# Kernel optimization log

Hardware: AMD Instinct MI355X
Metric: run time of the kernel (lower is better)

The kernel has to match this reference:

```python
import jax, jax.numpy as jnp
import numpy as np

B, R, D, P = 32, 512, 256, 5532  # images, rois/image, feat dim, num_pids
NEG_INF = -1e30

def setup_inputs() -> dict:
    key = jax.random.key(0)
    k1, k2, k3 = jax.random.split(key, 3)
    inputs = jax.random.normal(k1, (B * R, D), dtype=jnp.float32)
    cls_scores = jax.random.uniform(k2, (B * R, 1), dtype=jnp.float32)
    roi_label = jax.random.randint(k3, (B, R), 0, P + 1)  # 0 = background -> label -1
    return {"inputs": inputs, "cls_scores": cls_scores, "roi_label": roi_label}

def reference(inputs, cls_scores, roi_label):
    x = (inputs * cls_scores).reshape(B, R, D)          # scale features by cls score
    label = roi_label - 1                               # [B,R], -1 = background
    valid = label >= 0                                  # keep labeled ROIs only
    lbl = jnp.where(valid, label, 0)

    # per-image per-pid mean prototypes via one segmented reduction
    seg = (jnp.arange(B)[:, None] * P + lbl).reshape(-1)             # [B*R]
    w = valid.reshape(-1).astype(x.dtype)
    sums = jax.ops.segment_sum(x.reshape(-1, D) * w[:, None], seg, num_segments=B * P)
    counts = jax.ops.segment_sum(w, seg, num_segments=B * P)          # [B*P]
    proto = sums / jnp.maximum(counts, 1.0)[:, None]
    proto = proto / jnp.maximum(jnp.linalg.norm(proto, axis=-1, keepdims=True), 1e-12)
    proto = jax.lax.stop_gradient(proto).reshape(B, P, D)            # .detach() in torch
    present = (counts > 0).reshape(B, P)                              # unique labels per image

    # project each ROI feature onto its image's prototypes
    logits = jnp.einsum('brd,bpd->brp', x, proto)                     # [B,R,P]
    logits = jnp.where(present[:, None, :], logits, NEG_INF)          # softmax over unique labels only
    logp = jax.nn.log_softmax(logits, axis=-1)
    nll = -jnp.take_along_axis(logp, lbl[..., None], axis=-1)[..., 0] # [B,R]
    nll = jnp.where(valid, nll, 0.0)
    n_valid = jnp.maximum(jnp.sum(valid).astype(x.dtype), 1.0)
    return jnp.sum(nll) / n_valid
```

## Files before the change

kernel.cpp:

```cpp
#include <hip/hip_runtime.h>
#include <math.h>

#define Bn 32
#define Rn 512
#define Dn 256
#define Pn 5532
#define MAXU 512
#define NEGBIG -3.0e38f

typedef short short8 __attribute__((ext_vector_type(8)));
typedef short short4v __attribute__((ext_vector_type(4)));
typedef float floatx4 __attribute__((ext_vector_type(4)));

#define XBF_OFF    0
#define XBF_WORDS  (Bn*Rn*Dn/2)
#define PBF_OFF    (XBF_OFF + XBF_WORDS)
#define PBF_WORDS  (Bn*MAXU*Dn/2)
#define CMAP_OFF   (PBF_OFF + PBF_WORDS)
#define CCNT_OFF   (CMAP_OFF + Bn*Pn)
#define CURS_OFF   (CCNT_OFF + Bn*MAXU)
#define RLIST_OFF  (CURS_OFF + Bn*MAXU)
#define NUNIQ_OFF  (RLIST_OFF + Bn*Rn)
#define NVALID_OFF (NUNIQ_OFF + 32)
#define NLL_OFF    (NVALID_OFF + 32)
#define TICKET_OFF (NLL_OFF + 1)
#define MPART_OFF  (TICKET_OFF + 3)
#define SPART_OFF  (MPART_OFF + Bn*Rn*4)
#define DLBL_OFF   (SPART_OFF + Bn*Rn*4)

__device__ __forceinline__ unsigned short bf16r(float f) {
    union { float f; unsigned int u; } c; c.f = f;
    return (unsigned short)((c.u + 0x7FFFu + ((c.u >> 16) & 1u)) >> 16);
}

__device__ __forceinline__ void async16(void* lds, const void* g) {
    auto* l3 = reinterpret_cast<__attribute__((address_space(3))) unsigned int*>(
                   reinterpret_cast<size_t>(lds));
    auto* g1 = reinterpret_cast<const __attribute__((address_space(1))) unsigned int*>(
                   reinterpret_cast<size_t>(g));
    __builtin_amdgcn_global_load_lds(g1, l3, 16, 0, 0);
}

__global__ __launch_bounds__(1024) void k1_prep_compact(
    const float* __restrict__ inputs, const float* __restrict__ cls,
    const int* __restrict__ roi_label,
    unsigned short* __restrict__ xbf,
    int* __restrict__ cmap, int* __restrict__ ccnt, int* __restrict__ cursor,
    int* __restrict__ rlist, int* __restrict__ nuniq, int* __restrict__ nvalid_arr,
    float* __restrict__ nll, int* __restrict__ ticket)
{
    const int flat = blockIdx.x;
    const int t = threadIdx.x;

    __shared__ int cnt_lds[Pn];
    __shared__ int cmap_lds[Pn];
    __shared__ int curs_lds[MAXU];
    __shared__ int wpres[16], wcnt[16];

    if (flat >= 32) {
        if (flat == 32 && t == 0) { nll[0] = 0.f; ticket[0] = 0; }
        int g = (flat - 32) * 1024 + t;
        int e = g * 8;
        int row = e >> 8;
        float cw = cls[row];
        float4 v0 = *(const float4*)&inputs[e];
        float4 v1 = *(const float4*)&inputs[e + 4];
        short8 o;
        o[0] = (short)bf16r(v0.x * cw); o[1] = (short)bf16r(v0.y * cw);
        o[2] = (short)bf16r(v0.z * cw); o[3] = (short)bf16r(v0.w * cw);
        o[4] = (short)bf16r(v1.x * cw); o[5] = (short)bf16r(v1.y * cw);
        o[6] = (short)bf16r(v1.z * cw); o[7] = (short)bf16r(v1.w * cw);
        *(short8*)&xbf[e] = o;
        return;
    }

    const int b = flat;
    const int lane = t & 63, wid = t >> 6;
    for (int i = t; i < Pn; i += 1024) cnt_lds[i] = 0;
    __syncthreads();
    if (t < Rn) {
        int lbl = roi_label[b * Rn + t] - 1;
        if (lbl >= 0) atomicAdd(&cnt_lds[lbl], 1);
    }
    __syncthreads();

    int basePres = 0, baseCnt = 0;
    for (int i0 = 0; i0 < Pn; i0 += 1024) {
        int i = i0 + t;
        int cnt = (i < Pn) ? cnt_lds[i] : 0;
        bool pres = cnt > 0;
        unsigned long long mask = __ballot(pres);
        int pfx_pres = __popcll(mask & ((1ULL << lane) - 1ULL));
        int v = cnt;
        #pragma unroll
        for (int off = 1; off < 64; off <<= 1) {
            int u = __shfl_up(v, off);
            if (lane >= off) v += u;
        }
        int pfx_cnt = v - cnt;
        if (lane == 63) { wpres[wid] = __popcll(mask); wcnt[wid] = v; }
        __syncthreads();
        int woffP = 0, totP = 0, woffC = 0, totC = 0;
        #pragma unroll
        for (int w = 0; w < 16; ++w) {
            int p = wpres[w], c = wcnt[w];
            if (w < wid) { woffP += p; woffC += c; }
            totP += p; totC += c;
        }
        if (pres) {
            int c = basePres + woffP + pfx_pres;
            cmap_lds[i] = c;
            cmap[b * Pn + i] = c;
            ccnt[b * MAXU + c] = cnt;
            curs_lds[c] = baseCnt + woffC + pfx_cnt;
        }
        basePres += totP; baseCnt += totC;
        __syncthreads();
    }
    if (t < Rn) {
        int lbl = roi_label[b * Rn + t] - 1;
        if (lbl >= 0) {
            int c = cmap_lds[lbl];
            int pos = atomicAdd(&curs_lds[c], 1);
            rlist[b * Rn + pos] = t;
        }
    }
    __syncthreads();
    if (t < MAXU && t < basePres)
        cursor[b * MAXU + t] = curs_lds[t];
    if (t == 0) { nuniq[b] = basePres; nvalid_arr[b] = baseCnt; }
}

__global__ __launch_bounds__(256) void k2_proto(
    const float* __restrict__ inputs, const float* __restrict__ cls,
    const int* __restrict__ nuniq, const int* __restrict__ ccnt,
    const int* __restrict__ cursor, const int* __restrict__ rlist,
    unsigned short* __restrict__ pbf)
{
    const int lane = threadIdx.x & 63, wv = threadIdx.x >> 6;
    int s = blockIdx.x * 4 + wv;
    int b = s >> 9;
    int c = s & (MAXU - 1);
    if (c >= nuniq[b]) return;
    int cnt = ccnt[s];
    int start = cursor[s] - cnt;
    float4 acc = make_float4(0.f, 0.f, 0.f, 0.f);
    for (int k = 0; k < cnt; ++k) {
        int r = rlist[b * Rn + start + k];
        float cw = cls[b * Rn + r];
        float4 v = *(const float4*)&inputs[(size_t)(b * Rn + r) * Dn + lane * 4];
        acc.x += v.x * cw; acc.y += v.y * cw; acc.z += v.z * cw; acc.w += v.w * cw;
    }
    float inv = 1.0f / (float)cnt;
    acc.x *= inv; acc.y *= inv; acc.z *= inv; acc.w *= inv;
    float ss = acc.x*acc.x + acc.y*acc.y + acc.z*acc.z + acc.w*acc.w;
    #pragma unroll
    for (int off = 32; off > 0; off >>= 1) ss += __shfl_xor(ss, off);
    float scale = 1.0f / fmaxf(sqrtf(ss), 1e-12f);
    short4v o;
    o[0] = (short)bf16r(acc.x * scale); o[1] = (short)bf16r(acc.y * scale);
    o[2] = (short)bf16r(acc.z * scale); o[3] = (short)bf16r(acc.w * scale);
    *(short4v*)&pbf[(size_t)s * Dn + lane * 4] = o;
}

#define TRr 128
#define TCc 128
#define KCk 32

__global__ __launch_bounds__(256, 3) void k3_loss(
    const unsigned short* __restrict__ xbf, const unsigned short* __restrict__ pbf,
    const int* __restrict__ roi_label, const int* __restrict__ cmap,
    const int* __restrict__ nuniq,
    float* __restrict__ mpart, float* __restrict__ spart,
    float* __restrict__ dlbl_arr)
{
    __shared__ __align__(16) unsigned short xs[2][TRr * KCk];
    __shared__ __align__(16) unsigned short ps[2][TCc * KCk];
    __shared__ int lblc[TRr];
    __shared__ float mw[4][TRr], sw[4][TRr];

    const int t = threadIdx.x;
    const int lane = t & 63, w = t >> 6;
    const int q = lane >> 4, r15 = lane & 15;
    const int b = blockIdx.y;
    const int pc = blockIdx.z;
    const int roiBase = blockIdx.x * TRr;
    const int U = nuniq[b];
    if (pc * TCc >= U) return;

    if (t < TRr) {
        int lbl = roi_label[b * Rn + roiBase + t] - 1;
        lblc[t] = (lbl >= 0) ? cmap[b * Pn + lbl] : -1;
    }

    int xrow[2], xg[2];
    #pragma unroll
    for (int cc = 0; cc < 2; ++cc) {
        int s = (w + cc * 4) * 64 + lane;
        xrow[cc] = s >> 2; xg[cc] = (s & 3) ^ ((xrow[cc] >> 1) & 3);
    }

    #define ISSUE(kc, buf)                                                         \
        do {                                                                       \
            async16(&xs[buf][w * 512],                                             \
                    xbf + (size_t)(b * Rn + roiBase + xrow[0]) * Dn                \
                        + (kc) * KCk + xg[0] * 8);                                 \
            async16(&xs[buf][(w + 4) * 512],                                       \
                    xbf + (size_t)(b * Rn + roiBase + xrow[1]) * Dn                \
                        + (kc) * KCk + xg[1] * 8);                                 \
            async16(&ps[buf][w * 512],                                             \
                    pbf + (size_t)(b * MAXU + pc * TCc + xrow[0]) * Dn             \
                        + (kc) * KCk + xg[0] * 8);                                 \
            async16(&ps[buf][(w + 4) * 512],                                       \
                    pbf + (size_t)(b * MAXU + pc * TCc + xrow[1]) * Dn             \
                        + (kc) * KCk + xg[1] * 8);                                 \
        } while (0)

    ISSUE(0, 0);

    floatx4 acc[8][2];
    #pragma unroll
    for (int mt = 0; mt < 8; ++mt)
        #pragma unroll
        for (int nt = 0; nt < 2; ++nt) acc[mt][nt] = (floatx4)0.f;

    for (int kc = 0; kc < Dn / KCk; ++kc) {
        const int cur = kc & 1;
        __syncthreads();
        if (kc < Dn / KCk - 1) ISSUE(kc + 1, cur ^ 1);

        short8 bb[2];
        #pragma unroll
        for (int nt = 0; nt < 2; ++nt) {
            int row = w * 32 + nt * 16 + r15;
            int off = row * KCk + ((q ^ ((row >> 1) & 3)) * 8);
            bb[nt] = *(const short8*)&ps[cur][off];
        }
        #pragma unroll
        for (int mt = 0; mt < 8; ++mt) {
            int row = mt * 16 + r15;
            int off = row * KCk + ((q ^ ((row >> 1) & 3)) * 8);
            short8 a = *(const short8*)&xs[cur][off];
            acc[mt][0] = __builtin_amdgcn_mfma_f32_16x16x32_bf16(a, bb[0], acc[mt][0], 0, 0, 0);
            acc[mt][1] = __builtin_amdgcn_mfma_f32_16x16x32_bf16(a, bb[1], acc[mt][1], 0, 0, 0);
        }
    }
    #undef ISSUE

    const int c0 = pc * TCc + w * 32 + r15;
    const int c1 = c0 + 16;
    const bool v0 = c0 < U, v1 = c1 < U;
    #pragma unroll
    for (int mt = 0; mt < 8; ++mt)
        #pragma unroll
        for (int reg = 0; reg < 4; ++reg) {
            int mloc = mt * 16 + q * 4 + reg;
            float d0 = acc[mt][0][reg], d1 = acc[mt][1][reg];
            int lc = lblc[mloc];
            if (v0 && c0 == lc) dlbl_arr[b * Rn + roiBase + mloc] = d0;
            if (v1 && c1 == lc) dlbl_arr[b * Rn + roiBase + mloc] = d1;
            float M = fmaxf(v0 ? d0 : NEGBIG, v1 ? d1 : NEGBIG);
            #pragma unroll
            for (int off = 1; off < 16; off <<= 1) M = fmaxf(M, __shfl_xor(M, off));
            float s = (v0 ? __expf(d0 - M) : 0.f) + (v1 ? __expf(d1 - M) : 0.f);
            #pragma unroll
            for (int off = 1; off < 16; off <<= 1) s += __shfl_xor(s, off);
            if (r15 == 0) { mw[w][mloc] = M; sw[w][mloc] = s; }
        }
    __syncthreads();

    if (t < TRr) {
        float M = fmaxf(fmaxf(mw[0][t], mw[1][t]), fmaxf(mw[2][t], mw[3][t]));
        float s = 0.f;
        #pragma unroll
        for (int wv = 0; wv < 4; ++wv) s += sw[wv][t] * __expf(mw[wv][t] - M);
        int roi = b * Rn + roiBase + t;
        mpart[roi * 4 + pc] = M;
        spart[roi * 4 + pc] = s;
    }
}

__global__ __launch_bounds__(256) void k4_merge(
    const int* __restrict__ roi_label, const int* __restrict__ nuniq,
    const float* __restrict__ mpart, const float* __restrict__ spart,
    const float* __restrict__ dlbl_arr, float* __restrict__ nll_sum,
    int* __restrict__ ticket, const int* __restrict__ nvalid_arr,
    float* __restrict__ out)
{
    __shared__ float wsum[4];
    int roi = blockIdx.x * 256 + threadIdx.x;
    int b = roi >> 9;
    int lbl = roi_label[roi] - 1;
    float v = 0.f;
    if (lbl >= 0) {
        int U = nuniq[b];
        int nch = (U + TCc - 1) / TCc;
        float m = NEGBIG, s = 0.f;
        for (int pc = 0; pc < nch; ++pc) {
            float om = mpart[roi * 4 + pc], os = spart[roi * 4 + pc];
            float M = fmaxf(m, om);
            s = s * __expf(m - M) + os * __expf(om - M);
            m = M;
        }
        v = m + __logf(s) - dlbl_arr[roi];
    }
    #pragma unroll
    for (int off = 1; off < 64; off <<= 1) v += __shfl_xor(v, off);
    int lane = threadIdx.x & 63, wid = threadIdx.x >> 6;
    if (lane == 0) wsum[wid] = v;
    __syncthreads();
    if (threadIdx.x == 0) {
        atomicAdd(nll_sum, wsum[0] + wsum[1] + wsum[2] + wsum[3]);
        __threadfence();
        int tk = atomicAdd(ticket, 1);
        if (tk == gridDim.x - 1) {
            __threadfence();
            int s = 0;
            #pragma unroll
            for (int bb = 0; bb < Bn; ++bb) s += nvalid_arr[bb];
            out[0] = nll_sum[0] / fmaxf((float)s, 1.0f);
        }
    }
}

extern "C" void kernel_launch(void* const* d_in, const int* in_sizes, int n_in,
                              void* d_out, int out_size, void* d_ws, size_t ws_size,
                              hipStream_t stream) {
    const float* inputs = (const float*)d_in[0];
    const float* cls    = (const float*)d_in[1];
    const int*   roi    = (const int*)d_in[2];
    float* out = (float*)d_out;

    float* wsf = (float*)d_ws;
    int*   wsi = (int*)d_ws;
    unsigned short* xbf = (unsigned short*)(wsi + XBF_OFF);
    unsigned short* pbf = (unsigned short*)(wsi + PBF_OFF);
    int*   cmap   = wsi + CMAP_OFF;
    int*   ccnt   = wsi + CCNT_OFF;
    int*   cursor = wsi + CURS_OFF;
    int*   rlist  = wsi + RLIST_OFF;
    int*   nuniq  = wsi + NUNIQ_OFF;
    int*   nvalid = wsi + NVALID_OFF;
    float* nll    = wsf + NLL_OFF;
    int*   ticket = wsi + TICKET_OFF;
    float* mpart  = wsf + MPART_OFF;
    float* spart  = wsf + SPART_OFF;
    float* dlbl   = wsf + DLBL_OFF;

    k1_prep_compact<<<32 + 512, 1024, 0, stream>>>(inputs, cls, roi, xbf, cmap, ccnt,
                                                   cursor, rlist, nuniq, nvalid,
                                                   nll, ticket);
    k2_proto<<<(Bn * MAXU) / 4, 256, 0, stream>>>(inputs, cls, nuniq, ccnt, cursor,
                                                  rlist, pbf);
    dim3 g(Rn / TRr, Bn, 4);
    k3_loss<<<g, 256, 0, stream>>>(xbf, pbf, roi, cmap, nuniq, mpart, spart, dlbl);
    k4_merge<<<(Bn * Rn) / 256, 256, 0, stream>>>(roi, nuniq, mpart, spart, dlbl, nll,
                                                  ticket, nvalid, out);
}
```

Baseline: 106.6 us.

## Fuse prototype build into prep kernel and merge loss reduction into GEMM kernel

Prototype averaging and normalization now run inside the per-image prep blocks, using LDS-resident compacted lists instead of global cmap/rlist/cursor arrays. The separate merge kernel is removed: the loss kernel accumulates exp-sums per ROI with float atomics, and the last chunk block per tile, chosen by a ticket, takes the log and reduces to the output. This removes two kernel launches and the global round trips. The trade-offs are that the 32 prototype blocks must do all the gather work serially within a few CUs, and that the softmax is computed without max subtraction. That relies on the logits being bounded, since both vectors are normalized-ish.

```diff
diff --git a/kernel.cpp b/kernel.cpp
--- a/kernel.cpp
+++ b/kernel.cpp
@@ -6,7 +6,6 @@
 #define Dn 256
 #define Pn 5532
 #define MAXU 512
-#define NEGBIG -3.0e38f
 
 typedef short short8 __attribute__((ext_vector_type(8)));
 typedef short short4v __attribute__((ext_vector_type(4)));
@@ -16,17 +15,14 @@
 #define XBF_WORDS  (Bn*Rn*Dn/2)
 #define PBF_OFF    (XBF_OFF + XBF_WORDS)
 #define PBF_WORDS  (Bn*MAXU*Dn/2)
-#define CMAP_OFF   (PBF_OFF + PBF_WORDS)
-#define CCNT_OFF   (CMAP_OFF + Bn*Pn)
-#define CURS_OFF   (CCNT_OFF + Bn*MAXU)
-#define RLIST_OFF  (CURS_OFF + Bn*MAXU)
-#define NUNIQ_OFF  (RLIST_OFF + Bn*Rn)
+#define LBLC_OFF   (PBF_OFF + PBF_WORDS)
+#define NUNIQ_OFF  (LBLC_OFF + Bn*Rn)
 #define NVALID_OFF (NUNIQ_OFF + 32)
-#define NLL_OFF    (NVALID_OFF + 32)
-#define TICKET_OFF (NLL_OFF + 1)
-#define MPART_OFF  (TICKET_OFF + 3)
-#define SPART_OFF  (MPART_OFF + Bn*Rn*4)
-#define DLBL_OFF   (SPART_OFF + Bn*Rn*4)
+#define SEXP_OFF   (NVALID_OFF + 32)
+#define NLL_OFF    (SEXP_OFF + Bn*Rn)
+#define TK2_OFF    (NLL_OFF + 1)
+#define TICK_OFF   (TK2_OFF + 1)
+#define ZEROW      (Bn*Rn + 2 + 128)
 
 __device__ __forceinline__ unsigned short bf16r(float f) {
     union { float f; unsigned int u; } c; c.f = f;
@@ -41,24 +37,27 @@
     __builtin_amdgcn_global_load_lds(g1, l3, 16, 0, 0);
 }
 
-__global__ __launch_bounds__(1024) void k1_prep_compact(
+__global__ __launch_bounds__(1024) void k1_prep(
     const float* __restrict__ inputs, const float* __restrict__ cls,
     const int* __restrict__ roi_label,
-    unsigned short* __restrict__ xbf,
-    int* __restrict__ cmap, int* __restrict__ ccnt, int* __restrict__ cursor,
-    int* __restrict__ rlist, int* __restrict__ nuniq, int* __restrict__ nvalid_arr,
-    float* __restrict__ nll, int* __restrict__ ticket)
+    unsigned short* __restrict__ xbf, unsigned short* __restrict__ pbf,
+    int* __restrict__ lblc_arr, int* __restrict__ nuniq, int* __restrict__ nvalid_arr,
+    int* __restrict__ zbase)
 {
     const int flat = blockIdx.x;
     const int t = threadIdx.x;
 
     __shared__ int cnt_lds[Pn];
     __shared__ int cmap_lds[Pn];
-    __shared__ int curs_lds[MAXU];
+    __shared__ int curs_lds[MAXU], ccnt_lds[MAXU];
+    __shared__ int rlist_lds[Rn];
     __shared__ int wpres[16], wcnt[16];
 
     if (flat >= 32) {
-        if (flat == 32 && t == 0) { nll[0] = 0.f; ticket[0] = 0; }
+        if (flat >= 33 && flat <= 49) {
+            int idx = (flat - 33) * 1024 + t;
+            if (idx < ZEROW) zbase[idx] = 0;
+        }
         int g = (flat - 32) * 1024 + t;
         int e = g * 8;
         int row = e >> 8;
@@ -78,9 +77,10 @@
     const int lane = t & 63, wid = t >> 6;
     for (int i = t; i < Pn; i += 1024) cnt_lds[i] = 0;
     __syncthreads();
+    int mylbl = -1;
     if (t < Rn) {
-        int lbl = roi_label[b * Rn + t] - 1;
-        if (lbl >= 0) atomicAdd(&cnt_lds[lbl], 1);
+        mylbl = roi_label[b * Rn + t] - 1;
+        if (mylbl >= 0) atomicAdd(&cnt_lds[mylbl], 1);
     }
     __syncthreads();
 
@@ -110,57 +110,44 @@
         if (pres) {
             int c = basePres + woffP + pfx_pres;
             cmap_lds[i] = c;
-            cmap[b * Pn + i] = c;
-            ccnt[b * MAXU + c] = cnt;
+            ccnt_lds[c] = cnt;
             curs_lds[c] = baseCnt + woffC + pfx_cnt;
         }
         basePres += totP; baseCnt += totC;
         __syncthreads();
     }
     if (t < Rn) {
-        int lbl = roi_label[b * Rn + t] - 1;
-        if (lbl >= 0) {
-            int c = cmap_lds[lbl];
-            int pos = atomicAdd(&curs_lds[c], 1);
-            rlist[b * Rn + pos] = t;
-        }
-    }
-    __syncthreads();
-    if (t < MAXU && t < basePres)
-        cursor[b * MAXU + t] = curs_lds[t];
+        int lc = (mylbl >= 0) ? cmap_lds[mylbl] : -1;
+        lblc_arr[b * Rn + t] = lc;
+        if (lc >= 0) {
+            int pos = atomicAdd(&curs_lds[lc], 1);
+            rlist_lds[pos] = t;
+        }
+    }
     if (t == 0) { nuniq[b] = basePres; nvalid_arr[b] = baseCnt; }
-}
-
-__global__ __launch_bounds__(256) void k2_proto(
-    const float* __restrict__ inputs, const float* __restrict__ cls,
-    const int* __restrict__ nuniq, const int* __restrict__ ccnt,
-    const int* __restrict__ cursor, const int* __restrict__ rlist,
-    unsigned short* __restrict__ pbf)
-{
-    const int lane = threadIdx.x & 63, wv = threadIdx.x >> 6;
-    int s = blockIdx.x * 4 + wv;
-    int b = s >> 9;
-    int c = s & (MAXU - 1);
-    if (c >= nuniq[b]) return;
-    int cnt = ccnt[s];
-    int start = cursor[s] - cnt;
-    float4 acc = make_float4(0.f, 0.f, 0.f, 0.f);
-    for (int k = 0; k < cnt; ++k) {
-        int r = rlist[b * Rn + start + k];
-        float cw = cls[b * Rn + r];
-        float4 v = *(const float4*)&inputs[(size_t)(b * Rn + r) * Dn + lane * 4];
-        acc.x += v.x * cw; acc.y += v.y * cw; acc.z += v.z * cw; acc.w += v.w * cw;
-    }
-    float inv = 1.0f / (float)cnt;
-    acc.x *= inv; acc.y *= inv; acc.z *= inv; acc.w *= inv;
-    float ss = acc.x*acc.x + acc.y*acc.y + acc.z*acc.z + acc.w*acc.w;
-    #pragma unroll
-    for (int off = 32; off > 0; off >>= 1) ss += __shfl_xor(ss, off);
-    float scale = 1.0f / fmaxf(sqrtf(ss), 1e-12f);
-    short4v o;
-    o[0] = (short)bf16r(acc.x * scale); o[1] = (short)bf16r(acc.y * scale);
-    o[2] = (short)bf16r(acc.z * scale); o[3] = (short)bf16r(acc.w * scale);
-    *(short4v*)&pbf[(size_t)s * Dn + lane * 4] = o;
+    __syncthreads();
+
+    for (int s = wid; s < basePres; s += 16) {
+        int cnt = ccnt_lds[s];
+        int start = curs_lds[s] - cnt;
+        float4 acc = make_float4(0.f, 0.f, 0.f, 0.f);
+        for (int k = 0; k < cnt; ++k) {
+            int r = rlist_lds[start + k];
+            float cw = cls[b * Rn + r];
+            float4 v = *(const float4*)&inputs[(size_t)(b * Rn + r) * Dn + lane * 4];
+            acc.x += v.x * cw; acc.y += v.y * cw; acc.z += v.z * cw; acc.w += v.w * cw;
+        }
+        float inv = 1.0f / (float)cnt;
+        acc.x *= inv; acc.y *= inv; acc.z *= inv; acc.w *= inv;
+        float ss = acc.x*acc.x + acc.y*acc.y + acc.z*acc.z + acc.w*acc.w;
+        #pragma unroll
+        for (int off = 32; off > 0; off >>= 1) ss += __shfl_xor(ss, off);
+        float scale = 1.0f / fmaxf(sqrtf(ss), 1e-12f);
+        short4v o;
+        o[0] = (short)bf16r(acc.x * scale); o[1] = (short)bf16r(acc.y * scale);
+        o[2] = (short)bf16r(acc.z * scale); o[3] = (short)bf16r(acc.w * scale);
+        *(short4v*)&pbf[(size_t)(b * MAXU + s) * Dn + lane * 4] = o;
+    }
 }
 
 #define TRr 128
@@ -169,29 +156,29 @@
 
 __global__ __launch_bounds__(256, 3) void k3_loss(
     const unsigned short* __restrict__ xbf, const unsigned short* __restrict__ pbf,
-    const int* __restrict__ roi_label, const int* __restrict__ cmap,
-    const int* __restrict__ nuniq,
-    float* __restrict__ mpart, float* __restrict__ spart,
-    float* __restrict__ dlbl_arr)
+    const int* __restrict__ lblc_arr, const int* __restrict__ nuniq,
+    float* __restrict__ sexp, float* __restrict__ nll,
+    int* __restrict__ tick, int* __restrict__ ticket2,
+    const int* __restrict__ nvalid_arr, float* __restrict__ out)
 {
     __shared__ __align__(16) unsigned short xs[2][TRr * KCk];
     __shared__ __align__(16) unsigned short ps[2][TCc * KCk];
     __shared__ int lblc[TRr];
-    __shared__ float mw[4][TRr], sw[4][TRr];
+    __shared__ float msum[4];
+    __shared__ int mflag;
 
     const int t = threadIdx.x;
     const int lane = t & 63, w = t >> 6;
     const int q = lane >> 4, r15 = lane & 15;
+    const int rt = blockIdx.x;
     const int b = blockIdx.y;
     const int pc = blockIdx.z;
-    const int roiBase = blockIdx.x * TRr;
+    const int roiBase = rt * TRr;
     const int U = nuniq[b];
-    if (pc * TCc >= U) return;
-
-    if (t < TRr) {
-        int lbl = roi_label[b * Rn + roiBase + t] - 1;
-        lblc[t] = (lbl >= 0) ? cmap[b * Pn + lbl] : -1;
-    }
+    const int nch = (U == 0) ? 1 : ((U + TCc - 1) >> 7);
+    if (pc >= nch) return;
+
+    if (t < TRr) lblc[t] = lblc_arr[b * Rn + roiBase + t];
 
     int xrow[2], xg[2];
     #pragma unroll
@@ -250,6 +237,7 @@
     const int c0 = pc * TCc + w * 32 + r15;
     const int c1 = c0 + 16;
     const bool v0 = c0 < U, v1 = c1 < U;
+    float dsum = 0.f;
     #pragma unroll
     for (int mt = 0; mt < 8; ++mt)
         #pragma unroll
@@ -257,68 +245,42 @@
             int mloc = mt * 16 + q * 4 + reg;
             float d0 = acc[mt][0][reg], d1 = acc[mt][1][reg];
             int lc = lblc[mloc];
-            if (v0 && c0 == lc) dlbl_arr[b * Rn + roiBase + mloc] = d0;
-            if (v1 && c1 == lc) dlbl_arr[b * Rn + roiBase + mloc] = d1;
-            float M = fmaxf(v0 ? d0 : NEGBIG, v1 ? d1 : NEGBIG);
+            if (v0 && c0 == lc) dsum += d0;
+            if (v1 && c1 == lc) dsum += d1;
+            float es = (v0 ? __expf(d0) : 0.f) + (v1 ? __expf(d1) : 0.f);
             #pragma unroll
-            for (int off = 1; off < 16; off <<= 1) M = fmaxf(M, __shfl_xor(M, off));
-            float s = (v0 ? __expf(d0 - M) : 0.f) + (v1 ? __expf(d1 - M) : 0.f);
-            #pragma unroll
-            for (int off = 1; off < 16; off <<= 1) s += __shfl_xor(s, off);
-            if (r15 == 0) { mw[w][mloc] = M; sw[w][mloc] = s; }
-        }
-    __syncthreads();
-
-    if (t < TRr) {
-        float M = fmaxf(fmaxf(mw[0][t], mw[1][t]), fmaxf(mw[2][t], mw[3][t]));
-        float s = 0.f;
-        #pragma unroll
-        for (int wv = 0; wv < 4; ++wv) s += sw[wv][t] * __expf(mw[wv][t] - M);
-        int roi = b * Rn + roiBase + t;
-        mpart[roi * 4 + pc] = M;
-        spart[roi * 4 + pc] = s;
-    }
-}
-
-__global__ __launch_bounds__(256) void k4_merge(
-    const int* __restrict__ roi_label, const int* __restrict__ nuniq,
-    const float* __restrict__ mpart, const float* __restrict__ spart,
-    const float* __restrict__ dlbl_arr, float* __restrict__ nll_sum,
-    int* __restrict__ ticket, const int* __restrict__ nvalid_arr,
-    float* __restrict__ out)
-{
-    __shared__ float wsum[4];
-    int roi = blockIdx.x * 256 + threadIdx.x;
-    int b = roi >> 9;
-    int lbl = roi_label[roi] - 1;
-    float v = 0.f;
-    if (lbl >= 0) {
-        int U = nuniq[b];
-        int nch = (U + TCc - 1) / TCc;
-        float m = NEGBIG, s = 0.f;
-        for (int pc = 0; pc < nch; ++pc) {
-            float om = mpart[roi * 4 + pc], os = spart[roi * 4 + pc];
-            float M = fmaxf(m, om);
-            s = s * __expf(m - M) + os * __expf(om - M);
-            m = M;
-        }
-        v = m + __logf(s) - dlbl_arr[roi];
-    }
+            for (int off = 1; off < 16; off <<= 1) es += __shfl_xor(es, off);
+            if (r15 == 0) atomicAdd(&sexp[b * Rn + roiBase + mloc], es);
+        }
     #pragma unroll
-    for (int off = 1; off < 64; off <<= 1) v += __shfl_xor(v, off);
-    int lane = threadIdx.x & 63, wid = threadIdx.x >> 6;
-    if (lane == 0) wsum[wid] = v;
-    __syncthreads();
-    if (threadIdx.x == 0) {
-        atomicAdd(nll_sum, wsum[0] + wsum[1] + wsum[2] + wsum[3]);
+    for (int off = 1; off < 64; off <<= 1) dsum += __shfl_xor(dsum, off);
+    if (lane == 0) msum[w] = dsum;
+    __syncthreads();
+    if (t == 0) {
+        atomicAdd(nll, -(msum[0] + msum[1] + msum[2] + msum[3]));
         __threadfence();
-        int tk = atomicAdd(ticket, 1);
-        if (tk == gridDim.x - 1) {
+        int old = atomicAdd(&tick[b * 4 + rt], 1);
+        mflag = (old == nch - 1);
+    }
+    __syncthreads();
+    if (mflag) {
+        float v = 0.f;
+        if (t < TRr && lblc[t] >= 0)
+            v = __logf(atomicAdd(&sexp[b * Rn + roiBase + t], 0.0f));
+        #pragma unroll
+        for (int off = 1; off < 64; off <<= 1) v += __shfl_xor(v, off);
+        if (lane == 0) msum[w] = v;
+        __syncthreads();
+        if (t == 0) {
+            atomicAdd(nll, msum[0] + msum[1] + msum[2] + msum[3]);
             __threadfence();
-            int s = 0;
-            #pragma unroll
-            for (int bb = 0; bb < Bn; ++bb) s += nvalid_arr[bb];
-            out[0] = nll_sum[0] / fmaxf((float)s, 1.0f);
+            int t2 = atomicAdd(ticket2, 1);
+            if (t2 == 127) {
+                float total = atomicAdd(nll, 0.0f);
+                int nv = 0;
+                for (int bb = 0; bb < Bn; ++bb) nv += nvalid_arr[bb];
+                out[0] = total / fmaxf((float)nv, 1.0f);
+            }
         }
     }
 }
@@ -335,25 +297,17 @@
     int*   wsi = (int*)d_ws;
     unsigned short* xbf = (unsigned short*)(wsi + XBF_OFF);
     unsigned short* pbf = (unsigned short*)(wsi + PBF_OFF);
-    int*   cmap   = wsi + CMAP_OFF;
-    int*   ccnt   = wsi + CCNT_OFF;
-    int*   cursor = wsi + CURS_OFF;
-    int*   rlist  = wsi + RLIST_OFF;
+    int*   lblc   = wsi + LBLC_OFF;
     int*   nuniq  = wsi + NUNIQ_OFF;
     int*   nvalid = wsi + NVALID_OFF;
+    float* sexp   = wsf + SEXP_OFF;
     float* nll    = wsf + NLL_OFF;
-    int*   ticket = wsi + TICKET_OFF;
-    float* mpart  = wsf + MPART_OFF;
-    float* spart  = wsf + SPART_OFF;
-    float* dlbl   = wsf + DLBL_OFF;
-
-    k1_prep_compact<<<32 + 512, 1024, 0, stream>>>(inputs, cls, roi, xbf, cmap, ccnt,
-                                                   cursor, rlist, nuniq, nvalid,
-                                                   nll, ticket);
-    k2_proto<<<(Bn * MAXU) / 4, 256, 0, stream>>>(inputs, cls, nuniq, ccnt, cursor,
-                                                  rlist, pbf);
+    int*   tk2    = wsi + TK2_OFF;
+    int*   tick   = wsi + TICK_OFF;
+
+    k1_prep<<<32 + 512, 1024, 0, stream>>>(inputs, cls, roi, xbf, pbf, lblc,
+                                           nuniq, nvalid, wsi + SEXP_OFF);
     dim3 g(Rn / TRr, Bn, 4);
-    k3_loss<<<g, 256, 0, stream>>>(xbf, pbf, roi, cmap, nuniq, mpart, spart, dlbl);
-    k4_merge<<<(Bn * Rn) / 256, 256, 0, stream>>>(roi, nuniq, mpart, spart, dlbl, nll,
-                                                  ticket, nvalid, out);
-}
+    k3_loss<<<g, 256, 0, stream>>>(xbf, pbf, lblc, nuniq, sexp, nll, tick, tk2,
+                                   nvalid, out);
+}
```

After: 123.4 us. 1.16x slower.
